# Optimization experiments

Measured on AMD Instinct MI355X. Metric: run time of the kernel, lower is better.

Reference implementation:

```python
import jax, jax.numpy as jnp
import numpy as np

V, E, H, C = 50000, 300, 512, 3
B, P_LEN, H_LEN = 64, 128, 64


def _lstm(x, Wih, Whh, bih, bhh, h0, c0):
    """torch-style LSTM (gate order i,f,g,o). x: [B,T,E] -> outputs [B,T,H], hT, cT."""
    def step(carry, xt):
        h, c = carry
        g = xt @ Wih.T + h @ Whh.T + bih + bhh  # [B,4H]
        i, f, gg, o = jnp.split(g, 4, axis=-1)
        c = jax.nn.sigmoid(f) * c + jax.nn.sigmoid(i) * jnp.tanh(gg)
        h = jax.nn.sigmoid(o) * jnp.tanh(c)
        return (h, c), h
    (hT, cT), ys = jax.lax.scan(step, (h0, c0), jnp.swapaxes(x, 0, 1))
    return jnp.swapaxes(ys, 0, 1), hT, cT


def setup_inputs() -> dict:
    key = jax.random.key(0)
    ks = iter(jax.random.split(key, 32))
    n = lambda shape, s=0.05: jax.random.normal(next(ks), shape, dtype=jnp.float32) * s
    inp = {
        "premise": jax.random.randint(next(ks), (B, P_LEN), 0, V, dtype=jnp.int32),
        "hypothesis": jax.random.randint(next(ks), (B, H_LEN), 0, V, dtype=jnp.int32),
        "emb": n((V, E), 0.1),
        "Wih1": n((4 * H, E)), "Whh1": n((4 * H, H)), "bih1": n((4 * H,)), "bhh1": n((4 * H,)),
        "Wih2": n((4 * H, E)), "Whh2": n((4 * H, H)), "bih2": n((4 * H,)), "bhh2": n((4 * H,)),
        "W_y": n((H, H)), "W_h": n((H, H)), "W_r": n((H, H)), "W_t": n((H, H)),
        "w_att": n((1, H)),
        "fc1_w": n((H, H)), "fc1_b": n((H,)),
        "fc2_w": n((H, H)), "fc2_b": n((H,)),
        "fc3_w": n((C, H)), "fc3_b": n((C,)),
    }
    return inp


def reference(premise, hypothesis, emb,
              Wih1, Whh1, bih1, bhh1,
              Wih2, Whh2, bih2, bhh2,
              W_y, W_h, W_r, W_t, w_att,
              fc1_w, fc1_b, fc2_w, fc2_b, fc3_w, fc3_b):
    Bsz = premise.shape[0]
    Hd = Whh1.shape[1]
    zeros = jnp.zeros((Bsz, Hd), jnp.float32)

    # premise LSTM
    xp = emb[premise]                                   # [B,P,E]
    out_p, _, c_p = _lstm(xp, Wih1, Whh1, bih1, bhh1, zeros, zeros)
    # hypothesis LSTM initialized with (h0=0, c0=c_p)
    xh = emb[hypothesis]                                # [B,Th,E]
    out_h, hn_h, _ = _lstm(xh, Wih2, Whh2, bih2, bhh2, zeros, c_p)

    # word-by-word attention: a1 = W_y @ V^T, fixed across steps
    a1 = jnp.einsum('hj,bpj->bhp', W_y, out_p)          # [B,H,P]
    wv = w_att[0]                                       # [H]

    def att_step(r, q_t):
        # r: [B,H] attention state; q_t: [B,H] hypothesis step
        a2 = q_t @ W_h.T + r @ W_r.T                    # [B,H]
        s = jnp.einsum('h,bhp->bp', wv, jnp.tanh(a1 + a2[:, :, None]))
        scores = jax.nn.softmax(s, axis=-1)             # over premise positions
        r = jnp.einsum('bph,bp->bh', out_p, scores) + jnp.tanh(r @ W_t.T)
        return r, None

    r, _ = jax.lax.scan(att_step, zeros, jnp.swapaxes(out_h, 0, 1))

    rep = jnp.tanh(r @ fc1_w.T + fc1_b + hn_h @ fc2_w.T + fc2_b)
    return rep @ fc3_w.T + fc3_b                         # [B,C]
```

## Files before the change

kernel.cpp:

```cpp
#include <hip/hip_runtime.h>
#include <math.h>

#define BSZ 64
#define PLEN 128
#define HLEN 64
#define EDIM 300
#define HDIM 512
#define G4 2048
#define NCLS 3

#define TOFF 1000u
#define SPIN_CAP (1 << 18)

#define CR16 576
#define C16(f) ((((f) >> 5) * 36) + ((f) & 31))

__device__ __forceinline__ float sigf(float x) { return 1.0f / (1.0f + __expf(-x)); }
__device__ __forceinline__ float tanhfast(float x) { return 1.0f - 2.0f / (__expf(2.0f * x) + 1.0f); }

__device__ __forceinline__ unsigned long long aload64(const unsigned long long* p) {
    return __hip_atomic_load(p, __ATOMIC_RELAXED, __HIP_MEMORY_SCOPE_AGENT);
}
__device__ __forceinline__ void astore64(unsigned long long* p, unsigned long long v) {
    __hip_atomic_store(p, v, __ATOMIC_RELAXED, __HIP_MEMORY_SCOPE_AGENT);
}
__device__ __forceinline__ unsigned long long fpack2(float lo, float hi) {
    float2 v = make_float2(lo, hi);
    return *(unsigned long long*)&v;
}
__device__ __forceinline__ float2 funpack2(unsigned long long u) {
    union { unsigned long long u; float2 f; } c; c.u = u; return c.f;
}


__global__ __launch_bounds__(256) void ws_zero(unsigned long long* p) {
    p[(size_t)blockIdx.x * 256 + threadIdx.x] = 0ull;
}

__global__ __launch_bounds__(256) void proj_kernel(
    const int* __restrict__ toks, const float* __restrict__ emb,
    const float* __restrict__ Wih, const float* __restrict__ bih,
    const float* __restrict__ bhh, float* __restrict__ out)
{
    __shared__ float es[32 * 100];
    __shared__ float wsh[64 * 100];
    __shared__ int tks[32];
    const int m0 = blockIdx.x * 32, r0 = blockIdx.y * 64;
    const int tid = threadIdx.x;
    const int tx = tid & 15, ty = tid >> 4;
    float acc[2][4] = {{0.f, 0.f, 0.f, 0.f}, {0.f, 0.f, 0.f, 0.f}};
    if (tid < 32) tks[tid] = toks[m0 + tid];
    __syncthreads();
    for (int kc = 0; kc < 3; kc++) {
        if (kc) __syncthreads();
        for (int i = tid; i < 800; i += 256) {
            int row = i / 25, k4 = i % 25;
            ((float4*)es)[i] = ((const float4*)(emb + (size_t)tks[row] * EDIM + kc * 100))[k4];
        }
        for (int i = tid; i < 1600; i += 256) {
            int row = i / 25, k4 = i % 25;
            ((float4*)wsh)[i] = ((const float4*)(Wih + (size_t)(r0 + row) * EDIM + kc * 100))[k4];
        }
        __syncthreads();
        const float4* e0 = (const float4*)es + ty * 25;
        const float4* e1 = e0 + 16 * 25;
        const float4* w0 = (const float4*)wsh + tx * 25;
#pragma unroll
        for (int k = 0; k < 25; k++) {
            float4 ea = e0[k], eb = e1[k];
#pragma unroll
            for (int j = 0; j < 4; j++) {
                float4 w = w0[k + j * 400];
                acc[0][j] += ea.x * w.x + ea.y * w.y + ea.z * w.z + ea.w * w.w;
                acc[1][j] += eb.x * w.x + eb.y * w.y + eb.z * w.z + eb.w * w.w;
            }
        }
    }
#pragma unroll
    for (int j = 0; j < 4; j++) {
        int rr = r0 + tx + j * 16;
        float bsum = bih[rr] + bhh[rr];
        out[(size_t)(m0 + ty) * G4 + rr]      = acc[0][j] + bsum;
        out[(size_t)(m0 + ty + 16) * G4 + rr] = acc[1][j] + bsum;
    }
}

__global__ __launch_bounds__(256, 1) void lstm_coop(
    const float* __restrict__ xp, const float* __restrict__ xh,
    const float* __restrict__ Whh1, const float* __restrict__ Whh2,
    float* __restrict__ outp, float* __restrict__ outh,
    unsigned long long* __restrict__ hA, unsigned long long* __restrict__ hB,
    unsigned long long* __restrict__ hC, unsigned long long* __restrict__ hD,
    unsigned long long* __restrict__ doneH)
{
    const int tid = threadIdx.x;
    const int ug = blockIdx.x >> 3;
    const int bg = blockIdx.x & 7;
    const int u0 = ug * 16, b0 = bg * 8;
    const int rq = tid >> 4, cc = tid & 15;

    __shared__ __align__(16) float hst[8 * CR16];
    __shared__ float gsm[64][9];

    float4 w4[32];
#pragma unroll
    for (int j = 0; j < 4; j++) {
        int rr = 4 * rq + j;
        const float4* src = (const float4*)(Whh1 +
            ((size_t)((rr >> 4) * HDIM + u0 + (rr & 15))) * HDIM) + cc * 8;
#pragma unroll
        for (int q = 0; q < 8; q++) w4[j * 8 + q] = src[q];
    }
    float creg = 0.0f;
    const int bbc = tid >> 4, uuc = tid & 15;
    unsigned long long* dn = doneH + bg * 32;

    for (int t = 0; t < PLEN + HLEN; t++) {
        const int layer2 = (t >= PLEN) ? 1 : 0;
        const int tloc = layer2 ? t - PLEN : t;
        const int T = layer2 ? HLEN : PLEN;
        const float* xproj = layer2 ? xh : xp;
        float* outseq = layer2 ? outh : outp;
        unsigned long long* wA = layer2 ? hC : hA;
        unsigned long long* wB = layer2 ? hD : hB;
        unsigned long long* hwr = (t & 1) ? wB : wA;
        const unsigned long long* hrd = (t & 1) ? wA : wB;

        float gi = 0.f, gf = 0.f, gg = 0.f, go = 0.f;
        if (tid < 128) {
            size_t xb = ((size_t)(b0 + bbc) * T + tloc) * G4 + u0 + uuc;
            gi = xproj[xb];        gf = xproj[xb + 512];
            gg = xproj[xb + 1024]; go = xproj[xb + 1536];
        }

        if (t == PLEN) {
#pragma unroll
            for (int j = 0; j < 4; j++) {
                int rr = 4 * rq + j;
                const float4* src = (const float4*)(Whh2 +
                    ((size_t)((rr >> 4) * HDIM + u0 + (rr & 15))) * HDIM) + cc * 8;
#pragma unroll
                for (int q = 0; q < 8; q++) w4[j * 8 + q] = src[q];
            }
        }
        const bool have_h = (tloc != 0);
        if (have_h) {
            if (tid < 32) {
                unsigned long long v = aload64(dn + tid);
                int guard = 0;
                while (!__all(v >= (unsigned long long)t)) {
                    if (++guard > SPIN_CAP) break;
                    __builtin_amdgcn_s_sleep(1);
                    if (v < (unsigned long long)t) v = aload64(dn + tid);
                }
            }
            __syncthreads();
            __asm__ volatile("" ::: "memory");
            const unsigned long long* src = hrd + (size_t)b0 * 256;
            unsigned long long v[8];
#pragma unroll
            for (int i = 0; i < 8; i++) v[i] = aload64(src + tid + i * 256);
#pragma unroll
            for (int i = 0; i < 8; i++) {
                int idx = tid + i * 256;
                int bb = idx >> 8, j = idx & 255;
                float2 f = funpack2(v[i]);
                *(float2*)&hst[bb * CR16 + C16(2 * j)] = f;
            }
            __syncthreads();
#pragma unroll 1
            for (int bb = 0; bb < 8; bb++) {
                const float* hb = &hst[bb * CR16 + cc * 36];
                float a0 = 0.f, a1 = 0.f, a2 = 0.f, a3 = 0.f;
#pragma unroll
                for (int q = 0; q < 8; q++) {
                    float4 hv = *(const float4*)(hb + 4 * q);
                    float4 x;
                    x = w4[q];      a0 += x.x * hv.x + x.y * hv.y + x.z * hv.z + x.w * hv.w;
                    x = w4[8 + q];  a1 += x.x * hv.x + x.y * hv.y + x.z * hv.z + x.w * hv.w;
                    x = w4[16 + q]; a2 += x.x * hv.x + x.y * hv.y + x.z * hv.z + x.w * hv.w;
                    x = w4[24 + q]; a3 += x.x * hv.x + x.y * hv.y + x.z * hv.z + x.w * hv.w;
                }
#pragma unroll
                for (int o = 1; o < 16; o <<= 1) {
                    a0 += __shfl_xor(a0, o);
                    a1 += __shfl_xor(a1, o);
                    a2 += __shfl_xor(a2, o);
                    a3 += __shfl_xor(a3, o);
                }
                if (cc == 0) {
                    gsm[4 * rq + 0][bb] = a0;
                    gsm[4 * rq + 1][bb] = a1;
                    gsm[4 * rq + 2][bb] = a2;
                    gsm[4 * rq + 3][bb] = a3;
                }
            }
        }
        __syncthreads();
        float hn = 0.f;
        if (tid < 128) {
            if (have_h) {
                gi += gsm[uuc][bbc];
                gf += gsm[16 + uuc][bbc];
                gg += gsm[32 + uuc][bbc];
                go += gsm[48 + uuc][bbc];
            }
            float cn = sigf(gf) * creg + sigf(gi) * tanhfast(gg);
            hn = sigf(go) * tanhfast(cn);
            creg = cn;
            float pr = __shfl_xor(hn, 1);
            if ((uuc & 1) == 0)
                astore64(hwr + (size_t)(b0 + bbc) * 256 + (u0 + uuc) / 2, fpack2(hn, pr));
        }
        __asm__ volatile("s_waitcnt vmcnt(0)" ::: "memory");
        __syncthreads();
        if (tid == 0) astore64(&dn[ug], (unsigned long long)(t + 1));
        if (tid < 128)
            outseq[((size_t)(b0 + bbc) * T + tloc) * HDIM + u0 + uuc] = hn;
    }
}

__global__ __launch_bounds__(256) void a1_kernel(
    const float* __restrict__ Wy, const float* __restrict__ outp,
    float* __restrict__ a1t)
{
    __shared__ float os[32 * 132];
    __shared__ float wsh[64 * 132];
    const int b = blockIdx.x, p0 = blockIdx.y * 32, h0 = blockIdx.z * 64;
    const int tid = threadIdx.x;
    const int tx = tid & 15, ty = tid >> 4;
    float acc[2][4] = {{0.f, 0.f, 0.f, 0.f}, {0.f, 0.f, 0.f, 0.f}};
    for (int kc = 0; kc < 4; kc++) {
        if (kc) __syncthreads();
        for (int i = tid; i < 1024; i += 256) {
            int row = i >> 5, k4 = i & 31;
            ((float4*)os)[row * 33 + k4] =
                ((const float4*)(outp + ((size_t)(b * PLEN) + p0 + row) * HDIM + kc * 128))[k4];
        }
        for (int i = tid; i < 2048; i += 256) {
            int row = i >> 5, k4 = i & 31;
            ((float4*)wsh)[row * 33 + k4] =
                ((const float4*)(Wy + (size_t)(h0 + row) * HDIM + kc * 128))[k4];
        }
        __syncthreads();
        const float4* o0 = (const float4*)os + ty * 33;
        const float4* o1 = o0 + 16 * 33;
        const float4* w0 = (const float4*)wsh + tx * 33;
#pragma unroll
        for (int k = 0; k < 32; k++) {
            float4 ea = o0[k], eb = o1[k];
#pragma unroll
            for (int j = 0; j < 4; j++) {
                float4 w = w0[k + j * 528];
                acc[0][j] += ea.x * w.x + ea.y * w.y + ea.z * w.z + ea.w * w.w;
                acc[1][j] += eb.x * w.x + eb.y * w.y + eb.z * w.z + eb.w * w.w;
            }
        }
    }
#pragma unroll
    for (int j = 0; j < 4; j++) {
        int hh = h0 + tx + j * 16;
        a1t[((size_t)b * PLEN + p0 + ty) * HDIM + hh]      = acc[0][j];
        a1t[((size_t)b * PLEN + p0 + ty + 16) * HDIM + hh] = acc[1][j];
    }
}

#define OSTR 2056
__global__ __launch_bounds__(256, 1) void att_coop(
    const float* __restrict__ outh, const float* __restrict__ a1b,
    const float* __restrict__ outp,
    const float* __restrict__ Wh, const float* __restrict__ Wr,
    const float* __restrict__ Wt, const float* __restrict__ wv,
    unsigned long long* __restrict__ a2buf, unsigned long long* __restrict__ sbuf,
    unsigned long long* __restrict__ rA, unsigned long long* __restrict__ rB,
    unsigned long long* __restrict__ doneA, unsigned long long* __restrict__ doneB,
    unsigned long long* __restrict__ doneC)
{
    const int tid = threadIdx.x;
    const int ug = blockIdx.x >> 3;
    const int bg = blockIdx.x & 7;
    const int u0 = ug * 16, b0 = bg * 8;
    const int rq = tid >> 4, cc = tid & 15;
    const int m = rq >> 2;

    __shared__ __align__(16) float ops[8 * OSTR];
    __shared__ __align__(16) float qa[8 * CR16];
    __shared__ __align__(16) float rst[8 * CR16];
    __shared__ __align__(16) float scst[8][132];
    __shared__ float dsm[48][9];
    __shared__ float tts[16][9];
    __shared__ __align__(16) float wvs[512];

    float4 w4[32];
    if (rq < 12) {
        const float* W = (m == 0) ? Wh : ((m == 1) ? Wr : Wt);
#pragma unroll
        for (int j = 0; j < 4; j++) {
            int rr = 4 * rq + j;
            const float4* src = (const float4*)(W + (size_t)(u0 + (rr & 15)) * HDIM) + cc * 8;
#pragma unroll
            for (int q = 0; q < 8; q++) w4[j * 8 + q] = src[q];
        }
    }
    for (int i = tid; i < 128; i += 256)
        ((float4*)wvs)[i] = ((const float4*)wv)[i];

    for (int i = tid; i < 8 * 128 * 4; i += 256) {
        int bb = i >> 9;
        int rem = i & 511;
        int p = rem >> 2, q = rem & 3;
        float4 v = *((const float4*)(outp + ((size_t)(b0 + bb) * PLEN + p) * HDIM + u0) + q);
        *((float4*)(ops + bb * OSTR + p * 16) + q) = v;
    }

    const int wvid = tid >> 6, lane = tid & 63;
    const int p0g = ug * 4;
    float4 a1r[8][2];
#pragma unroll
    for (int i = 0; i < 8; i++) {
        int pr = wvid * 8 + i;
        int bb = pr >> 2, pp = pr & 3;
        const float4* src = (const float4*)(a1b + ((size_t)(b0 + bb) * PLEN + p0g + pp) * HDIM) + lane;
        a1r[i][0] = src[0];
        a1r[i][1] = src[64];
    }

    unsigned long long* dnA = doneA + bg * 32;
    unsigned long long* dnB = doneB + bg * 32;
    unsigned long long* dnC = doneC + bg * 32;
    const int bbc = tid >> 4, uuc = tid & 15;

    for (int t = 0; t < HLEN; t++) {
        unsigned long long* rwr = (t & 1) ? rB : rA;
        const unsigned long long* rrd = (t & 1) ? rA : rB;

        for (int i = tid; i < 8 * 128; i += 256) {
            int bb = i >> 7, k4 = i & 127;
            float4 v = ((const float4*)(outh + ((size_t)(b0 + bb) * HLEN + t) * HDIM))[k4];
            *(float4*)&qa[bb * CR16 + (k4 >> 3) * 36 + 4 * (k4 & 7)] = v;
        }
        if (t > 0) {
            const unsigned long long expt = TOFF + (unsigned long long)(3 * t);
            if (tid < 32) {
                unsigned long long v = aload64(dnC + tid);
                int guard = 0;
                while (!__all(v >= expt)) {
                    if (++guard > SPIN_CAP) break;
                    __builtin_amdgcn_s_sleep(1);
                    if (v < expt) v = aload64(dnC + tid);
                }
            }
            __syncthreads();
            __asm__ volatile("" ::: "memory");
            const unsigned long long* src = rrd + (size_t)b0 * 256;
            unsigned long long v[8];
#pragma unroll
            for (int i = 0; i < 8; i++) v[i] = aload64(src + tid + i * 256);
#pragma unroll
            for (int i = 0; i < 8; i++) {
                int idx = tid + i * 256;
                int bb = idx >> 8, j = idx & 255;
                float2 f = funpack2(v[i]);
                *(float2*)&rst[bb * CR16 + C16(2 * j)] = f;
            }
        }
        __syncthreads();
        if (rq < 12 && (t > 0 || m == 0)) {
#pragma unroll 1
            for (int bb = 0; bb < 8; bb++) {
                const float* svb = ((m == 0) ? &qa[bb * CR16] : &rst[bb * CR16]) + cc * 36;
                float a0 = 0.f, a1 = 0.f, a2 = 0.f, a3 = 0.f;
#pragma unroll
                for (int q = 0; q < 8; q++) {
                    float4 sv = *(const float4*)(svb + 4 * q);
                    float4 x;
                    x = w4[q];      a0 += x.x * sv.x + x.y * sv.y + x.z * sv.z + x.w * sv.w;
                    x = w4[8 + q];  a1 += x.x * sv.x + x.y * sv.y + x.z * sv.z + x.w * sv.w;
                    x = w4[16 + q]; a2 += x.x * sv.x + x.y * sv.y + x.z * sv.z + x.w * sv.w;
                    x = w4[24 + q]; a3 += x.x * sv.x + x.y * sv.y + x.z * sv.z + x.w * sv.w;
                }
#pragma unroll
                for (int o = 1; o < 16; o <<= 1) {
                    a0 += __shfl_xor(a0, o);
                    a1 += __shfl_xor(a1, o);
                    a2 += __shfl_xor(a2, o);
                    a3 += __shfl_xor(a3, o);
                }
                if (cc == 0) {
                    dsm[4 * rq + 0][bb] = a0;
                    dsm[4 * rq + 1][bb] = a1;
                    dsm[4 * rq + 2][bb] = a2;
                    dsm[4 * rq + 3][bb] = a3;
                }
            }
        }
        __syncthreads();
        if (tid < 128) {
            float aq = dsm[uuc][bbc];
            float ar = (t > 0) ? dsm[16 + uuc][bbc] : 0.0f;
            float at = (t > 0) ? dsm[32 + uuc][bbc] : 0.0f;
            float a2v = aq + ar;
            tts[uuc][bbc] = (t > 0) ? tanhfast(at) : 0.0f;
            float pr = __shfl_xor(a2v, 1);
            if ((uuc & 1) == 0)
                astore64(a2buf + (size_t)(b0 + bbc) * 256 + (u0 + uuc) / 2, fpack2(a2v, pr));
        }
        __asm__ volatile("s_waitcnt vmcnt(0)" ::: "memory");
        __syncthreads();
        if (tid == 0) astore64(&dnA[ug], TOFF + (unsigned long long)(3 * t + 1));

        {
            const unsigned long long expt = TOFF + (unsigned long long)(3 * t + 1);
            if (tid < 32) {
                unsigned long long v = aload64(dnA + tid);
                int guard = 0;
                while (!__all(v >= expt)) {
                    if (++guard > SPIN_CAP) break;
                    __builtin_amdgcn_s_sleep(1);
                    if (v < expt) v = aload64(dnA + tid);
                }
            }
            __syncthreads();
            __asm__ volatile("" ::: "memory");
            const unsigned long long* src = a2buf + (size_t)b0 * 256;
            unsigned long long v[8];
#pragma unroll
            for (int i = 0; i < 8; i++) v[i] = aload64(src + tid + i * 256);
#pragma unroll
            for (int i = 0; i < 8; i++) {
                int idx = tid + i * 256;
                int bb = idx >> 8, j = idx & 255;
                float2 f = funpack2(v[i]);
                *(float2*)&qa[bb * CR16 + C16(2 * j)] = f;
            }
        }
        __syncthreads();
        {
            float s8[8];
#pragma unroll 2
            for (int i = 0; i < 8; i++) {
                int pr = wvid * 8 + i;
                int bb = pr >> 2;
                float s = 0.f;
#pragma unroll
                for (int k = 0; k < 2; k++) {
                    int h4 = lane + 64 * k;
                    float4 av = a1r[i][k];
                    float4 a2v = *(const float4*)&qa[bb * CR16 + (h4 >> 3) * 36 + 4 * (h4 & 7)];
                    float4 wv4 = ((const float4*)wvs)[h4];
                    s += wv4.x * tanhfast(av.x + a2v.x)
                       + wv4.y * tanhfast(av.y + a2v.y)
                       + wv4.z * tanhfast(av.z + a2v.z)
                       + wv4.w * tanhfast(av.w + a2v.w);
                }
#pragma unroll
                for (int o = 1; o < 64; o <<= 1) s += __shfl_xor(s, o);
                s8[i] = s;
            }
            if (lane == 0) {
#pragma unroll
                for (int i = 0; i < 8; i += 2) {
                    int pr = wvid * 8 + i;
                    int bb = pr >> 2, pp = pr & 3;
                    astore64(sbuf + (size_t)(b0 + bb) * 64 + ug * 2 + (pp >> 1),
                             fpack2(s8[i], s8[i + 1]));
                }
            }
        }
        __asm__ volatile("s_waitcnt vmcnt(0)" ::: "memory");
        __syncthreads();
        if (tid == 0) astore64(&dnB[ug], TOFF + (unsigned long long)(3 * t + 2));

        {
            const unsigned long long expt = TOFF + (unsigned long long)(3 * t + 2);
            if (tid < 32) {
                unsigned long long v = aload64(dnB + tid);
                int guard = 0;
                while (!__all(v >= expt)) {
                    if (++guard > SPIN_CAP) break;
                    __builtin_amdgcn_s_sleep(1);
                    if (v < expt) v = aload64(dnB + tid);
                }
            }
            __syncthreads();
            __asm__ volatile("" ::: "memory");
            const unsigned long long* src = sbuf + (size_t)b0 * 64;
#pragma unroll
            for (int i = 0; i < 2; i++) {
                int idx = tid + i * 256;
                int bb = idx >> 6, j = idx & 63;
                float2 f = funpack2(aload64(src + bb * 64 + j));
                *(float2*)&scst[bb][2 * j] = f;
            }
        }
        __syncthreads();
        {
            const int bb = tid >> 5, j = tid & 31;
            float4 v = *(float4*)&scst[bb][j * 4];
            float mx = fmaxf(fmaxf(v.x, v.y), fmaxf(v.z, v.w));
#pragma unroll
            for (int o = 1; o < 32; o <<= 1) mx = fmaxf(mx, __shfl_xor(mx, o));
            float ex = __expf(v.x - mx), ey = __expf(v.y - mx);
            float ez = __expf(v.z - mx), ew = __expf(v.w - mx);
            float ssum = (ex + ey) + (ez + ew);
#pragma unroll
            for (int o = 1; o < 32; o <<= 1) ssum += __shfl_xor(ssum, o);
            float inv = 1.0f / ssum;
            float4 sc4 = make_float4(ex * inv, ey * inv, ez * inv, ew * inv);
            *(float4*)&scst[bb][j * 4] = sc4;
        }
        __syncthreads();
        if (tid < 128) {
            float acc = tts[uuc][bbc];
            const float* opb = ops + bbc * OSTR + uuc;
#pragma unroll 8
            for (int p = 0; p < PLEN; p++)
                acc += scst[bbc][p] * opb[p * 16];
            float pr = __shfl_xor(acc, 1);
            if ((uuc & 1) == 0)
                astore64(rwr + (size_t)(b0 + bbc) * 256 + (u0 + uuc) / 2, fpack2(acc, pr));
        }
        __asm__ volatile("s_waitcnt vmcnt(0)" ::: "memory");
        __syncthreads();
        if (tid == 0) astore64(&dnC[ug], TOFF + (unsigned long long)(3 * t + 3));
    }
}

__global__ __launch_bounds__(256) void final_kernel(
    const unsigned long long* __restrict__ r2, const float* __restrict__ outh,
    const float* __restrict__ fc1w, const float* __restrict__ fc1b,
    const float* __restrict__ fc2w, const float* __restrict__ fc2b,
    const float* __restrict__ fc3w, const float* __restrict__ fc3b,
    float* __restrict__ out)
{
    int b = blockIdx.x, tid = threadIdx.x;
    __shared__ float rs[HDIM], hs[HDIM], rep[HDIM], red[256];
    {
        float2 f = funpack2(r2[(size_t)b * 256 + tid]);
        rs[2 * tid] = f.x; rs[2 * tid + 1] = f.y;
    }
    for (int i = tid; i < 128; i += 256)
        ((float4*)hs)[i] = ((const float4*)(outh + ((size_t)(b * HLEN + HLEN - 1)) * HDIM))[i];
    __syncthreads();
    for (int u = tid; u < HDIM; u += 256) {
        const float4* w1 = (const float4*)(fc1w + (size_t)u * HDIM);
        const float4* w2 = (const float4*)(fc2w + (size_t)u * HDIM);
        float a = 0.f, bacc = 0.f;
        for (int k = 0; k < 128; k++) {
            float4 rv = ((float4*)rs)[k], hv = ((float4*)hs)[k];
            float4 x = w1[k]; a    += rv.x * x.x + rv.y * x.y + rv.z * x.z + rv.w * x.w;
            float4 y = w2[k]; bacc += hv.x * y.x + hv.y * y.y + hv.z * y.z + hv.w * y.w;
        }
        rep[u] = tanhfast(a + fc1b[u] + bacc + fc2b[u]);
    }
    __syncthreads();
    for (int cix = 0; cix < NCLS; cix++) {
        red[tid] = rep[tid] * fc3w[(size_t)cix * HDIM + tid]
                 + rep[tid + 256] * fc3w[(size_t)cix * HDIM + tid + 256];
        __syncthreads();
        for (int off = 128; off; off >>= 1) {
            if (tid < off) red[tid] += red[tid + off];
            __syncthreads();
        }
        if (tid == 0) out[b * NCLS + cix] = red[0] + fc3b[cix];
        __syncthreads();
    }
}

extern "C" void kernel_launch(void* const* d_in, const int* in_sizes, int n_in,
                              void* d_out, int out_size, void* d_ws, size_t ws_size,
                              hipStream_t stream)
{
    const int*   premise = (const int*)d_in[0];
    const int*   hyp     = (const int*)d_in[1];
    const float* emb     = (const float*)d_in[2];
    const float* Wih1    = (const float*)d_in[3];
    const float* Whh1    = (const float*)d_in[4];
    const float* bih1    = (const float*)d_in[5];
    const float* bhh1    = (const float*)d_in[6];
    const float* Wih2    = (const float*)d_in[7];
    const float* Whh2    = (const float*)d_in[8];
    const float* bih2    = (const float*)d_in[9];
    const float* bhh2    = (const float*)d_in[10];
    const float* Wy      = (const float*)d_in[11];
    const float* Wh      = (const float*)d_in[12];
    const float* Wr      = (const float*)d_in[13];
    const float* Wt      = (const float*)d_in[14];
    const float* wv      = (const float*)d_in[15];
    const float* fc1w    = (const float*)d_in[16];
    const float* fc1b    = (const float*)d_in[17];
    const float* fc2w    = (const float*)d_in[18];
    const float* fc2b    = (const float*)d_in[19];
    const float* fc3w    = (const float*)d_in[20];
    const float* fc3b    = (const float*)d_in[21];
    float* out = (float*)d_out;

    float* ws = (float*)d_ws;
    size_t off = 0;
    float* xp    = ws + off; off += (size_t)BSZ * PLEN * G4;
    float* xh    = ws + off; off += (size_t)BSZ * HLEN * G4;
    float* outp  = ws + off; off += (size_t)BSZ * PLEN * HDIM;
    float* outhp = ws + off; off += (size_t)BSZ * HLEN * HDIM;
    float* a1b   = ws + off; off += (size_t)BSZ * HDIM * PLEN;
    unsigned long long* tbase = (unsigned long long*)(ws + off);
    unsigned long long* hAb   = tbase;
    unsigned long long* hBb   = tbase + 16384;
    unsigned long long* hCb   = tbase + 2 * 16384;
    unsigned long long* hDb   = tbase + 3 * 16384;
    unsigned long long* a2b   = tbase + 4 * 16384;
    unsigned long long* sbb   = tbase + 5 * 16384;
    unsigned long long* dnH   = tbase + 5 * 16384 + 4096;
    unsigned long long* dnA   = dnH + 256;
    unsigned long long* dnB   = dnA + 256;
    unsigned long long* dnC   = dnB + 256;
    off += (size_t)(5 * 16384 + 4096 + 1024) * 2;
    if (ws_size < off * sizeof(float)) return;

    ws_zero<<<dim3(4), dim3(256), 0, stream>>>(dnH);

    proj_kernel<<<dim3(BSZ * PLEN / 32, G4 / 64), dim3(256), 0, stream>>>(
        premise, emb, Wih1, bih1, bhh1, xp);
    proj_kernel<<<dim3(BSZ * HLEN / 32, G4 / 64), dim3(256), 0, stream>>>(
        hyp, emb, Wih2, bih2, bhh2, xh);

    lstm_coop<<<dim3(256), dim3(256), 0, stream>>>(
        xp, xh, Whh1, Whh2, outp, outhp, hAb, hBb, hCb, hDb, dnH);

    a1_kernel<<<dim3(BSZ, PLEN / 32, HDIM / 64), dim3(256), 0, stream>>>(Wy, outp, a1b);

    att_coop<<<dim3(256), dim3(256), 0, stream>>>(
        outhp, a1b, outp, Wh, Wr, Wt, wv, a2b, sbb, hCb, hDb, dnA, dnB, dnC);

    final_kernel<<<dim3(BSZ), dim3(256), 0, stream>>>(
        hDb, outhp, fc1w, fc1b, fc2w, fc2b, fc3w, fc3b, out);
}
```

Before: 3.442 ms.

## Replace cooperative attention kernel with per-batch blocks and batched query projection

The cooperative attention kernel, which spread work across 256 blocks and synced them through global spin-wait flags three times per step, is replaced by one 512-thread block per batch element that runs all 64 steps with only block-level barriers. The hypothesis projection q_t @ W_h^T is hoisted out of the recurrence and computed for all steps at once by reusing the a1 GEMM kernel. This removes cross-block synchronisation latency. In exchange, only 64 blocks run, and each step streams Wr, Wt, a1 and out_p from global or cache memory instead of holding them in registers or shared memory.

Result: slower. 3.995 ms (+16.1%).

```diff
diff --git a/kernel.cpp b/kernel.cpp
--- a/kernel.cpp
+++ b/kernel.cpp
@@ -9,7 +9,6 @@
 #define G4 2048
 #define NCLS 3
 
-#define TOFF 1000u
 #define SPIN_CAP (1 << 18)
 
 #define CR16 576
@@ -31,7 +30,6 @@
 __device__ __forceinline__ float2 funpack2(unsigned long long u) {
     union { unsigned long long u; float2 f; } c; c.u = u; return c.f;
 }
-
 
 __global__ __launch_bounds__(256) void ws_zero(unsigned long long* p) {
     p[(size_t)blockIdx.x * 256 + threadIdx.x] = 0ull;
@@ -221,8 +219,8 @@
 }
 
 __global__ __launch_bounds__(256) void a1_kernel(
-    const float* __restrict__ Wy, const float* __restrict__ outp,
-    float* __restrict__ a1t)
+    const float* __restrict__ W, const float* __restrict__ src,
+    float* __restrict__ dst, int T)
 {
     __shared__ float os[32 * 132];
     __shared__ float wsh[64 * 132];
@@ -235,12 +233,12 @@
         for (int i = tid; i < 1024; i += 256) {
             int row = i >> 5, k4 = i & 31;
             ((float4*)os)[row * 33 + k4] =
-                ((const float4*)(outp + ((size_t)(b * PLEN) + p0 + row) * HDIM + kc * 128))[k4];
+                ((const float4*)(src + ((size_t)(b * T) + p0 + row) * HDIM + kc * 128))[k4];
         }
         for (int i = tid; i < 2048; i += 256) {
             int row = i >> 5, k4 = i & 31;
             ((float4*)wsh)[row * 33 + k4] =
-                ((const float4*)(Wy + (size_t)(h0 + row) * HDIM + kc * 128))[k4];
+                ((const float4*)(W + (size_t)(h0 + row) * HDIM + kc * 128))[k4];
         }
         __syncthreads();
         const float4* o0 = (const float4*)os + ty * 33;
@@ -260,274 +258,138 @@
 #pragma unroll
     for (int j = 0; j < 4; j++) {
         int hh = h0 + tx + j * 16;
-        a1t[((size_t)b * PLEN + p0 + ty) * HDIM + hh]      = acc[0][j];
-        a1t[((size_t)b * PLEN + p0 + ty + 16) * HDIM + hh] = acc[1][j];
-    }
-}
-
-#define OSTR 2056
-__global__ __launch_bounds__(256, 1) void att_coop(
-    const float* __restrict__ outh, const float* __restrict__ a1b,
+        dst[((size_t)b * T + p0 + ty) * HDIM + hh]      = acc[0][j];
+        dst[((size_t)b * T + p0 + ty + 16) * HDIM + hh] = acc[1][j];
+    }
+}
+
+__global__ __launch_bounds__(512, 1) void att_batch(
+    const float* __restrict__ a1b,
+    const float* __restrict__ a2qb,
     const float* __restrict__ outp,
-    const float* __restrict__ Wh, const float* __restrict__ Wr,
-    const float* __restrict__ Wt, const float* __restrict__ wv,
-    unsigned long long* __restrict__ a2buf, unsigned long long* __restrict__ sbuf,
-    unsigned long long* __restrict__ rA, unsigned long long* __restrict__ rB,
-    unsigned long long* __restrict__ doneA, unsigned long long* __restrict__ doneB,
-    unsigned long long* __restrict__ doneC)
-{
+    const float* __restrict__ Wr, const float* __restrict__ Wt,
+    const float* __restrict__ wv,
+    float* __restrict__ rout)
+{
+    const int b = blockIdx.x;
     const int tid = threadIdx.x;
-    const int ug = blockIdx.x >> 3;
-    const int bg = blockIdx.x & 7;
-    const int u0 = ug * 16, b0 = bg * 8;
-    const int rq = tid >> 4, cc = tid & 15;
-    const int m = rq >> 2;
-
-    __shared__ __align__(16) float ops[8 * OSTR];
-    __shared__ __align__(16) float qa[8 * CR16];
-    __shared__ __align__(16) float rst[8 * CR16];
-    __shared__ __align__(16) float scst[8][132];
-    __shared__ float dsm[48][9];
-    __shared__ float tts[16][9];
-    __shared__ __align__(16) float wvs[512];
-
-    float4 w4[32];
-    if (rq < 12) {
-        const float* W = (m == 0) ? Wh : ((m == 1) ? Wr : Wt);
-#pragma unroll
-        for (int j = 0; j < 4; j++) {
-            int rr = 4 * rq + j;
-            const float4* src = (const float4*)(W + (size_t)(u0 + (rr & 15)) * HDIM) + cc * 8;
-#pragma unroll
-            for (int q = 0; q < 8; q++) w4[j * 8 + q] = src[q];
-        }
-    }
-    for (int i = tid; i < 128; i += 256)
-        ((float4*)wvs)[i] = ((const float4*)wv)[i];
-
-    for (int i = tid; i < 8 * 128 * 4; i += 256) {
-        int bb = i >> 9;
-        int rem = i & 511;
-        int p = rem >> 2, q = rem & 3;
-        float4 v = *((const float4*)(outp + ((size_t)(b0 + bb) * PLEN + p) * HDIM + u0) + q);
-        *((float4*)(ops + bb * OSTR + p * 16) + q) = v;
-    }
-
-    const int wvid = tid >> 6, lane = tid & 63;
-    const int p0g = ug * 4;
-    float4 a1r[8][2];
-#pragma unroll
-    for (int i = 0; i < 8; i++) {
-        int pr = wvid * 8 + i;
-        int bb = pr >> 2, pp = pr & 3;
-        const float4* src = (const float4*)(a1b + ((size_t)(b0 + bb) * PLEN + p0g + pp) * HDIM) + lane;
-        a1r[i][0] = src[0];
-        a1r[i][1] = src[64];
-    }
-
-    unsigned long long* dnA = doneA + bg * 32;
-    unsigned long long* dnB = doneB + bg * 32;
-    unsigned long long* dnC = doneC + bg * 32;
-    const int bbc = tid >> 4, uuc = tid & 15;
+    const int g = tid >> 4, l = tid & 15;
+    const int pp = tid >> 3, tp = tid & 7;
+
+    __shared__ __align__(16) float rsh[512];
+    __shared__ __align__(16) float a2sh[512];
+    __shared__ __align__(16) float ttsh[512];
+    __shared__ __align__(16) float wvsh[512];
+    __shared__ float ssh[128];
+    __shared__ float scsh[128];
+    __shared__ float red[4];
+
+    const float* a1base = a1b + (size_t)b * 128 * 512;
+    const float* opbase = outp + (size_t)b * 128 * 512;
+    const float* a2qbase = a2qb + (size_t)b * 64 * 512;
+
+    wvsh[tid] = wv[tid];
+    rsh[tid] = 0.f;
+    __syncthreads();
 
     for (int t = 0; t < HLEN; t++) {
-        unsigned long long* rwr = (t & 1) ? rB : rA;
-        const unsigned long long* rrd = (t & 1) ? rA : rB;
-
-        for (int i = tid; i < 8 * 128; i += 256) {
-            int bb = i >> 7, k4 = i & 127;
-            float4 v = ((const float4*)(outh + ((size_t)(b0 + bb) * HLEN + t) * HDIM))[k4];
-            *(float4*)&qa[bb * CR16 + (k4 >> 3) * 36 + 4 * (k4 & 7)] = v;
-        }
+        a2sh[tid] = a2qbase[(size_t)t * 512 + tid];
+        float4 rv[8];
         if (t > 0) {
-            const unsigned long long expt = TOFF + (unsigned long long)(3 * t);
-            if (tid < 32) {
-                unsigned long long v = aload64(dnC + tid);
-                int guard = 0;
-                while (!__all(v >= expt)) {
-                    if (++guard > SPIN_CAP) break;
-                    __builtin_amdgcn_s_sleep(1);
-                    if (v < expt) v = aload64(dnC + tid);
-                }
-            }
-            __syncthreads();
-            __asm__ volatile("" ::: "memory");
-            const unsigned long long* src = rrd + (size_t)b0 * 256;
-            unsigned long long v[8];
-#pragma unroll
-            for (int i = 0; i < 8; i++) v[i] = aload64(src + tid + i * 256);
-#pragma unroll
-            for (int i = 0; i < 8; i++) {
-                int idx = tid + i * 256;
-                int bb = idx >> 8, j = idx & 255;
-                float2 f = funpack2(v[i]);
-                *(float2*)&rst[bb * CR16 + C16(2 * j)] = f;
-            }
-        }
-        __syncthreads();
-        if (rq < 12 && (t > 0 || m == 0)) {
+#pragma unroll
+            for (int kk = 0; kk < 8; kk++)
+                rv[kk] = *(const float4*)&rsh[4 * l + 64 * kk];
+        }
+        __syncthreads();
+        if (t > 0) {
 #pragma unroll 1
-            for (int bb = 0; bb < 8; bb++) {
-                const float* svb = ((m == 0) ? &qa[bb * CR16] : &rst[bb * CR16]) + cc * 36;
-                float a0 = 0.f, a1 = 0.f, a2 = 0.f, a3 = 0.f;
-#pragma unroll
-                for (int q = 0; q < 8; q++) {
-                    float4 sv = *(const float4*)(svb + 4 * q);
-                    float4 x;
-                    x = w4[q];      a0 += x.x * sv.x + x.y * sv.y + x.z * sv.z + x.w * sv.w;
-                    x = w4[8 + q];  a1 += x.x * sv.x + x.y * sv.y + x.z * sv.z + x.w * sv.w;
-                    x = w4[16 + q]; a2 += x.x * sv.x + x.y * sv.y + x.z * sv.z + x.w * sv.w;
-                    x = w4[24 + q]; a3 += x.x * sv.x + x.y * sv.y + x.z * sv.z + x.w * sv.w;
+            for (int j = 0; j < 16; j++) {
+                const int u = g * 16 + j;
+                const float4* wr = (const float4*)(Wr + (size_t)u * 512) + l;
+                const float4* wt = (const float4*)(Wt + (size_t)u * 512) + l;
+                float ar = 0.f, at = 0.f;
+#pragma unroll
+                for (int kk = 0; kk < 8; kk++) {
+                    float4 w1 = wr[16 * kk];
+                    float4 w2 = wt[16 * kk];
+                    float4 r4 = rv[kk];
+                    ar += w1.x * r4.x + w1.y * r4.y + w1.z * r4.z + w1.w * r4.w;
+                    at += w2.x * r4.x + w2.y * r4.y + w2.z * r4.z + w2.w * r4.w;
                 }
 #pragma unroll
                 for (int o = 1; o < 16; o <<= 1) {
-                    a0 += __shfl_xor(a0, o);
-                    a1 += __shfl_xor(a1, o);
-                    a2 += __shfl_xor(a2, o);
-                    a3 += __shfl_xor(a3, o);
-                }
-                if (cc == 0) {
-                    dsm[4 * rq + 0][bb] = a0;
-                    dsm[4 * rq + 1][bb] = a1;
-                    dsm[4 * rq + 2][bb] = a2;
-                    dsm[4 * rq + 3][bb] = a3;
-                }
-            }
-        }
-        __syncthreads();
+                    ar += __shfl_xor(ar, o);
+                    at += __shfl_xor(at, o);
+                }
+                if (l == 0) {
+                    a2sh[u] += ar;
+                    ttsh[u] = tanhfast(at);
+                }
+            }
+        } else {
+            ttsh[tid] = 0.f;
+        }
+        __syncthreads();
+
+#pragma unroll
+        for (int pass = 0; pass < 2; pass++) {
+            const int p = pass * 64 + pp;
+            const float* a1p = a1base + (size_t)p * 512;
+            float s = 0.f;
+#pragma unroll
+            for (int i = 0; i < 16; i++) {
+                const int h0 = 4 * tp + 32 * i;
+                float4 av = *(const float4*)(a1p + h0);
+                float4 a2v = *(const float4*)&a2sh[h0];
+                float4 wv4 = *(const float4*)&wvsh[h0];
+                s += wv4.x * tanhfast(av.x + a2v.x)
+                   + wv4.y * tanhfast(av.y + a2v.y)
+                   + wv4.z * tanhfast(av.z + a2v.z)
+                   + wv4.w * tanhfast(av.w + a2v.w);
+            }
+#pragma unroll
+            for (int o = 1; o < 8; o <<= 1) s += __shfl_xor(s, o);
+            if (tp == 0) ssh[p] = s;
+        }
+        __syncthreads();
+
+        float e = 0.f;
         if (tid < 128) {
-            float aq = dsm[uuc][bbc];
-            float ar = (t > 0) ? dsm[16 + uuc][bbc] : 0.0f;
-            float at = (t > 0) ? dsm[32 + uuc][bbc] : 0.0f;
-            float a2v = aq + ar;
-            tts[uuc][bbc] = (t > 0) ? tanhfast(at) : 0.0f;
-            float pr = __shfl_xor(a2v, 1);
-            if ((uuc & 1) == 0)
-                astore64(a2buf + (size_t)(b0 + bbc) * 256 + (u0 + uuc) / 2, fpack2(a2v, pr));
-        }
-        __asm__ volatile("s_waitcnt vmcnt(0)" ::: "memory");
-        __syncthreads();
-        if (tid == 0) astore64(&dnA[ug], TOFF + (unsigned long long)(3 * t + 1));
-
+            float s = ssh[tid];
+            float m = s;
+#pragma unroll
+            for (int o = 1; o < 64; o <<= 1) m = fmaxf(m, __shfl_xor(m, o));
+            if ((tid & 63) == 0) red[tid >> 6] = m;
+        }
+        __syncthreads();
+        if (tid < 128) {
+            float mx = fmaxf(red[0], red[1]);
+            e = __expf(ssh[tid] - mx);
+            float sm = e;
+#pragma unroll
+            for (int o = 1; o < 64; o <<= 1) sm += __shfl_xor(sm, o);
+            if ((tid & 63) == 0) red[2 + (tid >> 6)] = sm;
+        }
+        __syncthreads();
+        if (tid < 128) scsh[tid] = e / (red[2] + red[3]);
+        __syncthreads();
+
+        float acc = ttsh[tid];
         {
-            const unsigned long long expt = TOFF + (unsigned long long)(3 * t + 1);
-            if (tid < 32) {
-                unsigned long long v = aload64(dnA + tid);
-                int guard = 0;
-                while (!__all(v >= expt)) {
-                    if (++guard > SPIN_CAP) break;
-                    __builtin_amdgcn_s_sleep(1);
-                    if (v < expt) v = aload64(dnA + tid);
-                }
-            }
-            __syncthreads();
-            __asm__ volatile("" ::: "memory");
-            const unsigned long long* src = a2buf + (size_t)b0 * 256;
-            unsigned long long v[8];
-#pragma unroll
-            for (int i = 0; i < 8; i++) v[i] = aload64(src + tid + i * 256);
-#pragma unroll
-            for (int i = 0; i < 8; i++) {
-                int idx = tid + i * 256;
-                int bb = idx >> 8, j = idx & 255;
-                float2 f = funpack2(v[i]);
-                *(float2*)&qa[bb * CR16 + C16(2 * j)] = f;
-            }
-        }
-        __syncthreads();
-        {
-            float s8[8];
-#pragma unroll 2
-            for (int i = 0; i < 8; i++) {
-                int pr = wvid * 8 + i;
-                int bb = pr >> 2;
-                float s = 0.f;
-#pragma unroll
-                for (int k = 0; k < 2; k++) {
-                    int h4 = lane + 64 * k;
-                    float4 av = a1r[i][k];
-                    float4 a2v = *(const float4*)&qa[bb * CR16 + (h4 >> 3) * 36 + 4 * (h4 & 7)];
-                    float4 wv4 = ((const float4*)wvs)[h4];
-                    s += wv4.x * tanhfast(av.x + a2v.x)
-                       + wv4.y * tanhfast(av.y + a2v.y)
-                       + wv4.z * tanhfast(av.z + a2v.z)
-                       + wv4.w * tanhfast(av.w + a2v.w);
-                }
-#pragma unroll
-                for (int o = 1; o < 64; o <<= 1) s += __shfl_xor(s, o);
-                s8[i] = s;
-            }
-            if (lane == 0) {
-#pragma unroll
-                for (int i = 0; i < 8; i += 2) {
-                    int pr = wvid * 8 + i;
-                    int bb = pr >> 2, pp = pr & 3;
-                    astore64(sbuf + (size_t)(b0 + bb) * 64 + ug * 2 + (pp >> 1),
-                             fpack2(s8[i], s8[i + 1]));
-                }
-            }
-        }
-        __asm__ volatile("s_waitcnt vmcnt(0)" ::: "memory");
-        __syncthreads();
-        if (tid == 0) astore64(&dnB[ug], TOFF + (unsigned long long)(3 * t + 2));
-
-        {
-            const unsigned long long expt = TOFF + (unsigned long long)(3 * t + 2);
-            if (tid < 32) {
-                unsigned long long v = aload64(dnB + tid);
-                int guard = 0;
-                while (!__all(v >= expt)) {
-                    if (++guard > SPIN_CAP) break;
-                    __builtin_amdgcn_s_sleep(1);
-                    if (v < expt) v = aload64(dnB + tid);
-                }
-            }
-            __syncthreads();
-            __asm__ volatile("" ::: "memory");
-            const unsigned long long* src = sbuf + (size_t)b0 * 64;
-#pragma unroll
-            for (int i = 0; i < 2; i++) {
-                int idx = tid + i * 256;
-                int bb = idx >> 6, j = idx & 63;
-                float2 f = funpack2(aload64(src + bb * 64 + j));
-                *(float2*)&scst[bb][2 * j] = f;
-            }
-        }
-        __syncthreads();
-        {
-            const int bb = tid >> 5, j = tid & 31;
-            float4 v = *(float4*)&scst[bb][j * 4];
-            float mx = fmaxf(fmaxf(v.x, v.y), fmaxf(v.z, v.w));
-#pragma unroll
-            for (int o = 1; o < 32; o <<= 1) mx = fmaxf(mx, __shfl_xor(mx, o));
-            float ex = __expf(v.x - mx), ey = __expf(v.y - mx);
-            float ez = __expf(v.z - mx), ew = __expf(v.w - mx);
-            float ssum = (ex + ey) + (ez + ew);
-#pragma unroll
-            for (int o = 1; o < 32; o <<= 1) ssum += __shfl_xor(ssum, o);
-            float inv = 1.0f / ssum;
-            float4 sc4 = make_float4(ex * inv, ey * inv, ez * inv, ew * inv);
-            *(float4*)&scst[bb][j * 4] = sc4;
-        }
-        __syncthreads();
-        if (tid < 128) {
-            float acc = tts[uuc][bbc];
-            const float* opb = ops + bbc * OSTR + uuc;
+            const float* op = opbase + tid;
 #pragma unroll 8
-            for (int p = 0; p < PLEN; p++)
-                acc += scst[bbc][p] * opb[p * 16];
-            float pr = __shfl_xor(acc, 1);
-            if ((uuc & 1) == 0)
-                astore64(rwr + (size_t)(b0 + bbc) * 256 + (u0 + uuc) / 2, fpack2(acc, pr));
-        }
-        __asm__ volatile("s_waitcnt vmcnt(0)" ::: "memory");
-        __syncthreads();
-        if (tid == 0) astore64(&dnC[ug], TOFF + (unsigned long long)(3 * t + 3));
+            for (int p = 0; p < 128; p++)
+                acc += scsh[p] * op[(size_t)p * 512];
+        }
+        __syncthreads();
+        rsh[tid] = acc;
+        if (t == HLEN - 1) rout[(size_t)b * 512 + tid] = acc;
+        __syncthreads();
     }
 }
 
 __global__ __launch_bounds__(256) void final_kernel(
-    const unsigned long long* __restrict__ r2, const float* __restrict__ outh,
+    const float* __restrict__ r, const float* __restrict__ outh,
     const float* __restrict__ fc1w, const float* __restrict__ fc1b,
     const float* __restrict__ fc2w, const float* __restrict__ fc2b,
     const float* __restrict__ fc3w, const float* __restrict__ fc3b,
@@ -535,12 +397,10 @@
 {
     int b = blockIdx.x, tid = threadIdx.x;
     __shared__ float rs[HDIM], hs[HDIM], rep[HDIM], red[256];
-    {
-        float2 f = funpack2(r2[(size_t)b * 256 + tid]);
-        rs[2 * tid] = f.x; rs[2 * tid + 1] = f.y;
-    }
-    for (int i = tid; i < 128; i += 256)
+    for (int i = tid; i < 128; i += 256) {
+        ((float4*)rs)[i] = ((const float4*)(r + (size_t)b * HDIM))[i];
         ((float4*)hs)[i] = ((const float4*)(outh + ((size_t)(b * HLEN + HLEN - 1)) * HDIM))[i];
+    }
     __syncthreads();
     for (int u = tid; u < HDIM; u += 256) {
         const float4* w1 = (const float4*)(fc1w + (size_t)u * HDIM);
@@ -602,21 +462,18 @@
     float* outp  = ws + off; off += (size_t)BSZ * PLEN * HDIM;
     float* outhp = ws + off; off += (size_t)BSZ * HLEN * HDIM;
     float* a1b   = ws + off; off += (size_t)BSZ * HDIM * PLEN;
+    float* a2qb  = xp;
+    float* rout  = xh;
     unsigned long long* tbase = (unsigned long long*)(ws + off);
     unsigned long long* hAb   = tbase;
     unsigned long long* hBb   = tbase + 16384;
     unsigned long long* hCb   = tbase + 2 * 16384;
     unsigned long long* hDb   = tbase + 3 * 16384;
-    unsigned long long* a2b   = tbase + 4 * 16384;
-    unsigned long long* sbb   = tbase + 5 * 16384;
-    unsigned long long* dnH   = tbase + 5 * 16384 + 4096;
-    unsigned long long* dnA   = dnH + 256;
-    unsigned long long* dnB   = dnA + 256;
-    unsigned long long* dnC   = dnB + 256;
-    off += (size_t)(5 * 16384 + 4096 + 1024) * 2;
+    unsigned long long* dnH   = tbase + 4 * 16384;
+    off += (size_t)(4 * 16384 + 256) * 2;
     if (ws_size < off * sizeof(float)) return;
 
-    ws_zero<<<dim3(4), dim3(256), 0, stream>>>(dnH);
+    ws_zero<<<dim3(1), dim3(256), 0, stream>>>(dnH);
 
     proj_kernel<<<dim3(BSZ * PLEN / 32, G4 / 64), dim3(256), 0, stream>>>(
         premise, emb, Wih1, bih1, bhh1, xp);
@@ -626,11 +483,14 @@
     lstm_coop<<<dim3(256), dim3(256), 0, stream>>>(
         xp, xh, Whh1, Whh2, outp, outhp, hAb, hBb, hCb, hDb, dnH);
 
-    a1_kernel<<<dim3(BSZ, PLEN / 32, HDIM / 64), dim3(256), 0, stream>>>(Wy, outp, a1b);
-
-    att_coop<<<dim3(256), dim3(256), 0, stream>>>(
-        outhp, a1b, outp, Wh, Wr, Wt, wv, a2b, sbb, hCb, hDb, dnA, dnB, dnC);
+    a1_kernel<<<dim3(BSZ, PLEN / 32, HDIM / 64), dim3(256), 0, stream>>>(
+        Wy, outp, a1b, PLEN);
+    a1_kernel<<<dim3(BSZ, HLEN / 32, HDIM / 64), dim3(256), 0, stream>>>(
+        Wh, outhp, a2qb, HLEN);
+
+    att_batch<<<dim3(BSZ), dim3(512), 0, stream>>>(
+        a1b, a2qb, outp, Wr, Wt, wv, rout);
 
     final_kernel<<<dim3(BSZ), dim3(256), 0, stream>>>(
-        hDb, outhp, fc1w, fc1b, fc2w, fc2b, fc3w, fc3b, out);
-}
+        rout, outhp, fc1w, fc1b, fc2w, fc2b, fc3w, fc3b, out);
+}
```
